# Kernel optimization log

Measured on AMD Instinct MI355X. Metric: run time of the kernel, lower is better.

The kernel has to match this reference:

```python
import jax, jax.numpy as jnp
import numpy as np
import math

B, NOUT, NCLASSES, CENTER, TOPK = 1024, 512, 5994, 3, 5
M, SUB_M, SCALE = 0.2, -0.06, 30.0

COS_M, SIN_M = math.cos(M), math.sin(M)
TH, MM = math.cos(math.pi - M), math.sin(math.pi - M) * M
SUB_COS_M, SUB_SIN_M = math.cos(SUB_M), math.sin(SUB_M)
SUB_TH, SUB_MM = math.cos(math.pi - SUB_M), math.sin(math.pi - SUB_M) * SUB_M


def setup_inputs() -> dict:
    key = jax.random.key(0)
    k1, k2, k3 = jax.random.split(key, 3)
    x = jax.random.normal(k1, (B, NOUT), dtype=jnp.float32)
    # xavier_normal over (center, nClasses, nOut): fan_in=nClasses*nOut, fan_out=center*nOut
    std = math.sqrt(2.0 / (NCLASSES * NOUT + CENTER * NOUT))
    weight = jax.random.normal(k2, (CENTER, NCLASSES, NOUT), dtype=jnp.float32) * std
    label = jax.random.randint(k3, (B,), 0, NCLASSES, dtype=jnp.int64)
    return {"x": x, "weight": weight, "label": label}


def _l2norm(v, axis=-1, eps=1e-12):
    return v / jnp.maximum(jnp.linalg.norm(v, axis=axis, keepdims=True), eps)


def reference(x, weight, label):
    xn = _l2norm(x)                       # [B, j]
    wn = _l2norm(weight)                  # [a, c, j]
    cosine_subcen = jnp.einsum('bj,acj->bac', xn, wn)   # [B, center, C]
    cosine = jnp.max(cosine_subcen, axis=1)             # [B, C]

    sine = jnp.sqrt(jnp.clip(1.0 - cosine * cosine, 0.0, 1.0))
    phi = jnp.where(cosine - TH > 0, cosine * COS_M - sine * SIN_M, cosine - MM)
    sub_phi = jnp.where(cosine - SUB_TH > 0,
                        cosine * SUB_COS_M - sine * SUB_SIN_M,
                        cosine - SUB_MM)

    # topk+1 candidates; drop the label column if present, else drop the last
    _, idx = jax.lax.top_k(cosine, TOPK + 1)            # [B, topk+1]
    is_label = (idx == label[:, None].astype(idx.dtype))
    # stable sort pushes the (unique) label hit to the end, preserving order otherwise
    order = jnp.argsort(is_label.astype(jnp.int32), axis=1, stable=True)
    idx_fixed = jnp.take_along_axis(idx, order[:, :TOPK], axis=1)   # [B, topk]

    rows = jnp.arange(B)[:, None]
    one_hot_sub = jnp.zeros_like(cosine).at[rows, idx_fixed].add(1.0)
    one_hot = jax.nn.one_hot(label, NCLASSES, dtype=cosine.dtype)

    output = (one_hot * phi + one_hot_sub * sub_phi
              + (1.0 - one_hot_sub - one_hot) * cosine) * SCALE

    logp = jax.nn.log_softmax(output, axis=-1)
    loss = -jnp.mean(logp[jnp.arange(B), label])

    pred = jnp.argmax(cosine * SCALE, axis=-1)
    prec1 = jnp.mean((pred == label).astype(jnp.float32)) * 100.0
    return loss, prec1
```

## Files before the change

kernel.cpp:

```cpp
#include <hip/hip_runtime.h>
#include <math.h>

#define NB 1024
#define NC 5994
#define NCP 6016
#define NK 512
#define NA 3
#define NT 48
#define SCALE_F 30.0f
#define NPT 24

#define COS_M_F 0.9800665778412416f
#define SIN_M_F 0.19866933079506122f
#define TH_F (-0.9800665778412416f)
#define MM_F 0.039733866159012244f
#define SUB_COS_M_F 0.9982005399352042f
#define SUB_SIN_M_F (-0.05996400647944459f)
#define SUB_TH_F (-0.9982005399352042f)
#define SUB_MM_F 0.0035978403887666754f

typedef __attribute__((ext_vector_type(8))) short short8;
typedef __attribute__((ext_vector_type(4))) float f32x4;

__device__ __forceinline__ float waveReduceSum(float v) {
#pragma unroll
  for (int off = 32; off > 0; off >>= 1) v += __shfl_down(v, off);
  return v;
}

__device__ __forceinline__ void waveArgMax(float& v, int& i) {
#pragma unroll
  for (int off = 32; off > 0; off >>= 1) {
    float ov = __shfl_down(v, off);
    int oi = __shfl_down(i, off);
    if (ov > v || (ov == v && (unsigned)oi < (unsigned)i)) { v = ov; i = oi; }
  }
}

__device__ __forceinline__ ushort f2bf(float f) {
  unsigned u = __float_as_uint(f);
  u += 0x7FFFu + ((u >> 16) & 1u);
  return (ushort)(u >> 16);
}

__device__ __forceinline__ void load_lds16(const ushort* g, ushort* l) {
  __builtin_amdgcn_global_load_lds(
      (const __attribute__((address_space(1))) unsigned int*)g,
      (__attribute__((address_space(3))) unsigned int*)l, 16, 0, 0);
}

__global__ __launch_bounds__(256) void norm_convert(const float* __restrict__ x,
                                                    const float* __restrict__ w,
                                                    ushort* __restrict__ xb,
                                                    ushort* __restrict__ wb) {
  const int row = blockIdx.x * 4 + (threadIdx.x >> 6);
  const int lane = threadIdx.x & 63;
  const float* src;
  ushort* dst;
  if (row < NB) {
    src = x + (size_t)row * NK;
    dst = xb + (size_t)row * NK;
  } else {
    const int r = row - NB;
    const int a = r / NCP, c = r % NCP;
    dst = wb + (size_t)r * NK;
    if (c >= NC) {
      ushort4 z = {0, 0, 0, 0};
      *(ushort4*)(dst + lane * 4) = z;
      *(ushort4*)(dst + 256 + lane * 4) = z;
      return;
    }
    src = w + ((size_t)a * NC + c) * NK;
  }
  const float4 v0 = *(const float4*)(src + lane * 4);
  const float4 v1 = *(const float4*)(src + 256 + lane * 4);
  float ss = v0.x * v0.x + v0.y * v0.y + v0.z * v0.z + v0.w * v0.w +
             v1.x * v1.x + v1.y * v1.y + v1.z * v1.z + v1.w * v1.w;
  ss = waveReduceSum(ss);
  ss = __shfl(ss, 0);
  const float rn = 1.0f / fmaxf(sqrtf(ss), 1e-12f);
  ushort4 o0 = {f2bf(v0.x * rn), f2bf(v0.y * rn), f2bf(v0.z * rn), f2bf(v0.w * rn)};
  ushort4 o1 = {f2bf(v1.x * rn), f2bf(v1.y * rn), f2bf(v1.z * rn), f2bf(v1.w * rn)};
  *(ushort4*)(dst + lane * 4) = o0;
  *(ushort4*)(dst + 256 + lane * 4) = o1;
}

__global__ __launch_bounds__(256) void cos_gemm_mfma(const ushort* __restrict__ Xb,
                                                     const ushort* __restrict__ Wb,
                                                     float* __restrict__ cosine) {
  __shared__ ushort sA0[128 * 32];
  __shared__ ushort sA1[128 * 32];
  __shared__ ushort sB0[128 * 32];
  __shared__ ushort sB1[128 * 32];
  const int tid = threadIdx.x;
  const int lane = tid & 63;
  const int w = tid >> 6;
  const int wr = w >> 1, wc = w & 1;
  const int b0 = blockIdx.y * 128;
  const int c0 = blockIdx.x * 128;

  const int e0 = w * 2;
  const int srow = e0 * 16 + (lane >> 2);
  const int scol = (lane & 3) * 8;
  const ushort* gA = Xb + (size_t)(b0 + srow) * NK + scol;
  const ushort* gB = Wb + (size_t)(c0 + srow) * NK + scol;
  const int lds0 = e0 * 512;
  const int lds1 = (e0 + 1) * 512;

  const int r = lane & 15;
  const int kg = lane >> 4;
  const int offA = (wr * 64 + r) * 32 + kg * 8;
  const int offB = (wc * 64 + r) * 32 + kg * 8;

  f32x4 best[4][4];
  f32x4 acc[4][4];
#pragma unroll
  for (int i = 0; i < 4; ++i)
#pragma unroll
    for (int j = 0; j < 4; ++j) {
#pragma unroll
      for (int q = 0; q < 4; ++q) best[i][j][q] = -INFINITY;
      acc[i][j] = (f32x4)(0.f);
    }

  load_lds16(gA, (ushort*)sA0 + lds0);
  load_lds16(gA + 16 * NK, (ushort*)sA0 + lds1);
  load_lds16(gB, (ushort*)sB0 + lds0);
  load_lds16(gB + 16 * NK, (ushort*)sB0 + lds1);
  __syncthreads();

#define GEMM_BODY(T, SAr, SBr, SAw, SBw)                                        \
  {                                                                             \
    const int t_ = (T);                                                         \
    if (t_ + 1 < NT) {                                                          \
      const int tn = t_ + 1;                                                    \
      const int k0 = (tn & 15) << 5;                                            \
      const size_t boff = (size_t)(tn >> 4) * NCP * NK;                         \
      load_lds16(gA + k0, (ushort*)SAw + lds0);                                 \
      load_lds16(gA + k0 + 16 * NK, (ushort*)SAw + lds1);                       \
      load_lds16(gB + boff + k0, (ushort*)SBw + lds0);                          \
      load_lds16(gB + boff + k0 + 16 * NK, (ushort*)SBw + lds1);                \
    }                                                                           \
    short8 af[4], bf[4];                                                        \
    _Pragma("unroll") for (int mi = 0; mi < 4; ++mi)                            \
        af[mi] = *(const short8*)&SAr[offA + mi * 512];                         \
    _Pragma("unroll") for (int ni = 0; ni < 4; ++ni)                            \
        bf[ni] = *(const short8*)&SBr[offB + ni * 512];                         \
    _Pragma("unroll") for (int mi = 0; mi < 4; ++mi)                            \
        _Pragma("unroll") for (int ni = 0; ni < 4; ++ni)                        \
            acc[mi][ni] = __builtin_amdgcn_mfma_f32_16x16x32_bf16(              \
                af[mi], bf[ni], acc[mi][ni], 0, 0, 0);                          \
    if ((t_ & 15) == 15) {                                                      \
      _Pragma("unroll") for (int i = 0; i < 4; ++i)                             \
          _Pragma("unroll") for (int j = 0; j < 4; ++j) {                       \
        _Pragma("unroll") for (int q = 0; q < 4; ++q)                           \
            best[i][j][q] = fmaxf(best[i][j][q], acc[i][j][q]);                 \
        acc[i][j] = (f32x4)(0.f);                                               \
      }                                                                         \
    }                                                                           \
    __syncthreads();                                                            \
  }

  for (int t = 0; t < NT; t += 2) {
    GEMM_BODY(t, sA0, sB0, sA1, sB1)
    GEMM_BODY(t + 1, sA1, sB1, sA0, sB0)
  }
#undef GEMM_BODY

  const int q4 = (lane >> 4) * 4;
#pragma unroll
  for (int ni = 0; ni < 4; ++ni) {
    const int col = c0 + wc * 64 + ni * 16 + r;
    if (col < NC) {
#pragma unroll
      for (int mi = 0; mi < 4; ++mi) {
        const int row0 = b0 + wr * 64 + mi * 16 + q4;
#pragma unroll
        for (int q = 0; q < 4; ++q)
          cosine[(size_t)(row0 + q) * NC + col] = best[mi][ni][q];
      }
    }
  }
}

__global__ __launch_bounds__(256) void row_loss(const float* __restrict__ cosine,
                                                const int* __restrict__ label,
                                                float* __restrict__ loss_b,
                                                float* __restrict__ corr_b) {
  __shared__ float swv[4];
  __shared__ int swi[4];
  __shared__ float s_red[4];
  __shared__ float s_maxv;
  __shared__ float s_cosL;
  __shared__ float topv[6];
  __shared__ int topi[6];

  const int b = blockIdx.x, tid = threadIdx.x;
  const int wv = tid >> 6;
  const int lab = label[b];
  const float* row = cosine + (size_t)b * NC;

  float v[NPT];
  float bv = -INFINITY;
  int bi = -1;
#pragma unroll
  for (int j = 0; j < NPT; ++j) {
    const int i = tid + j * 256;
    v[j] = (i < NC) ? row[i] : -INFINITY;
    if (v[j] > bv) { bv = v[j]; bi = i; }
  }
  if (tid == (lab & 255)) s_cosL = v[lab >> 8];
  waveArgMax(bv, bi);
  if ((tid & 63) == 0) { swv[wv] = bv; swi[wv] = bi; }
  __syncthreads();
  if (tid == 0) {
    float mv = swv[0]; int mi = swi[0];
    for (int q = 1; q < 4; ++q)
      if (swv[q] > mv || (swv[q] == mv && (unsigned)swi[q] < (unsigned)mi)) { mv = swv[q]; mi = swi[q]; }
    s_maxv = mv; topv[0] = mv; topi[0] = mi;
  }
  __syncthreads();
  const float maxv = s_maxv;

  float ps = 0.f;
#pragma unroll
  for (int j = 0; j < NPT; ++j) ps += __expf(SCALE_F * (v[j] - maxv));
  ps = waveReduceSum(ps);
  if ((tid & 63) == 0) s_red[wv] = ps;

  unsigned excl = 0;
  {
    const int wi = topi[0];
    if ((wi & 255) == tid) excl |= 1u << (wi >> 8);
  }

  for (int e = 1; e < 6; ++e) {
    float lv = -INFINITY;
    int li = -1;
#pragma unroll
    for (int j = 0; j < NPT; ++j)
      if (!((excl >> j) & 1u) && v[j] > lv) { lv = v[j]; li = tid + j * 256; }
    waveArgMax(lv, li);
    if ((tid & 63) == 0) { swv[wv] = lv; swi[wv] = li; }
    __syncthreads();
    if (tid == 0) {
      float mv = swv[0]; int mi = swi[0];
      for (int q = 1; q < 4; ++q)
        if (swv[q] > mv || (swv[q] == mv && (unsigned)swi[q] < (unsigned)mi)) { mv = swv[q]; mi = swi[q]; }
      topv[e] = mv; topi[e] = mi;
    }
    __syncthreads();
    const int wi = topi[e];
    if ((wi & 255) == tid) excl |= 1u << (wi >> 8);
  }

  if (tid == 0) {
    const float S = s_red[0] + s_red[1] + s_red[2] + s_red[3];
    const float m = SCALE_F * maxv;
    const float cosL = s_cosL;
    const float sineL = sqrtf(fminf(fmaxf(1.f - cosL * cosL, 0.f), 1.f));
    const float phiL = (cosL - TH_F > 0.f) ? (cosL * COS_M_F - sineL * SIN_M_F) : (cosL - MM_F);
    float adj = __expf(SCALE_F * phiL - m) - __expf(SCALE_F * cosL - m);
    int cnt = 0;
    for (int e = 0; e < 6 && cnt < 5; ++e) {
      if (topi[e] == lab) continue;
      const float c = topv[e];
      const float sine = sqrtf(fminf(fmaxf(1.f - c * c, 0.f), 1.f));
      const float sp = (c - SUB_TH_F > 0.f) ? (c * SUB_COS_M_F - sine * SUB_SIN_M_F) : (c - SUB_MM_F);
      adj += __expf(SCALE_F * sp - m) - __expf(SCALE_F * c - m);
      ++cnt;
    }
    const float Sp = S + adj;
    loss_b[b] = (logf(Sp) + m) - SCALE_F * phiL;
    corr_b[b] = (topi[0] == lab) ? 1.f : 0.f;
  }
}

__global__ __launch_bounds__(256) void finalize(const float* __restrict__ loss_b,
                                                const float* __restrict__ corr_b,
                                                float* __restrict__ out) {
  const int tid = threadIdx.x;
  float ls = 0.f, cs = 0.f;
  for (int i = tid; i < NB; i += 256) { ls += loss_b[i]; cs += corr_b[i]; }
  ls = waveReduceSum(ls);
  cs = waveReduceSum(cs);
  __shared__ float sl[4], sc[4];
  if ((tid & 63) == 0) { sl[tid >> 6] = ls; sc[tid >> 6] = cs; }
  __syncthreads();
  if (tid == 0) {
    const float L = sl[0] + sl[1] + sl[2] + sl[3];
    const float Cr = sc[0] + sc[1] + sc[2] + sc[3];
    out[0] = L / (float)NB;
    out[1] = Cr / (float)NB * 100.f;
  }
}

extern "C" void kernel_launch(void* const* d_in, const int* in_sizes, int n_in,
                              void* d_out, int out_size, void* d_ws, size_t ws_size,
                              hipStream_t stream) {
  const float* x = (const float*)d_in[0];
  const float* w = (const float*)d_in[1];
  const int* label = (const int*)d_in[2];
  float* out = (float*)d_out;
  char* ws = (char*)d_ws;

  ushort* xb = (ushort*)ws;
  ushort* wb = (ushort*)(ws + 1048576);
  float* cosine = (float*)(ws + 1048576 + 18481152);
  float* loss_b = (float*)(ws + 1048576 + 18481152 + 24551424);
  float* corr_b = loss_b + NB;

  norm_convert<<<(NB + NA * NCP) / 4, 256, 0, stream>>>(x, w, xb, wb);
  cos_gemm_mfma<<<dim3(NCP / 128, NB / 128), 256, 0, stream>>>(xb, wb, cosine);
  row_loss<<<NB, 256, 0, stream>>>(cosine, label, loss_b, corr_b);
  finalize<<<1, 256, 0, stream>>>(loss_b, corr_b, out);
}
```

Before: 71.90 us.

## Use 512-thread GEMM blocks with swizzled 1D grid and padded classes

The GEMM block grows to 8 waves, each now computing a 32x64 sub-tile instead of 64x64, which halves per-thread accumulators and staging loads. Class padding becomes 6144 so the grid is exactly 48x8 tiles. Blocks are remapped from a 1D grid so that groups of 8 column tiles share row tiles, aimed at better L2 reuse. Loss scratch buffers now reuse the xb workspace region, which is dead by the time row_loss runs. The aim is more latency hiding and fewer registers, at the cost of extra padded rows in normalization and GEMM.

```diff
diff --git a/kernel.cpp b/kernel.cpp
--- a/kernel.cpp
+++ b/kernel.cpp
@@ -3,7 +3,9 @@
 
 #define NB 1024
 #define NC 5994
-#define NCP 6016
+#define NCP 6144
+#define NCX 48
+#define NBY 8
 #define NK 512
 #define NA 3
 #define NT 48
@@ -85,7 +87,7 @@
   *(ushort4*)(dst + 256 + lane * 4) = o1;
 }
 
-__global__ __launch_bounds__(256) void cos_gemm_mfma(const ushort* __restrict__ Xb,
+__global__ __launch_bounds__(512) void cos_gemm_mfma(const ushort* __restrict__ Xb,
                                                      const ushort* __restrict__ Wb,
                                                      float* __restrict__ cosine) {
   __shared__ ushort sA0[128 * 32];
@@ -96,26 +98,30 @@
   const int lane = tid & 63;
   const int w = tid >> 6;
   const int wr = w >> 1, wc = w & 1;
-  const int b0 = blockIdx.y * 128;
-  const int c0 = blockIdx.x * 128;
-
-  const int e0 = w * 2;
-  const int srow = e0 * 16 + (lane >> 2);
+
+  const int id = blockIdx.x;
+  const int resid = id & 7;
+  const int by = (id >> 3) & 7;
+  const int chunk = id >> 6;
+  const int cx = chunk * 8 + resid;
+  const int b0 = by * 128;
+  const int c0 = cx * 128;
+
+  const int srow = w * 16 + (lane >> 2);
   const int scol = (lane & 3) * 8;
   const ushort* gA = Xb + (size_t)(b0 + srow) * NK + scol;
   const ushort* gB = Wb + (size_t)(c0 + srow) * NK + scol;
-  const int lds0 = e0 * 512;
-  const int lds1 = (e0 + 1) * 512;
+  const int ldsw = w * 512;
 
   const int r = lane & 15;
   const int kg = lane >> 4;
-  const int offA = (wr * 64 + r) * 32 + kg * 8;
+  const int offA = (wr * 32 + r) * 32 + kg * 8;
   const int offB = (wc * 64 + r) * 32 + kg * 8;
 
-  f32x4 best[4][4];
-  f32x4 acc[4][4];
-#pragma unroll
-  for (int i = 0; i < 4; ++i)
+  f32x4 best[2][4];
+  f32x4 acc[2][4];
+#pragma unroll
+  for (int i = 0; i < 2; ++i)
 #pragma unroll
     for (int j = 0; j < 4; ++j) {
 #pragma unroll
@@ -123,10 +129,8 @@
       acc[i][j] = (f32x4)(0.f);
     }
 
-  load_lds16(gA, (ushort*)sA0 + lds0);
-  load_lds16(gA + 16 * NK, (ushort*)sA0 + lds1);
-  load_lds16(gB, (ushort*)sB0 + lds0);
-  load_lds16(gB + 16 * NK, (ushort*)sB0 + lds1);
+  load_lds16(gA, (ushort*)sA0 + ldsw);
+  load_lds16(gB, (ushort*)sB0 + ldsw);
   __syncthreads();
 
 #define GEMM_BODY(T, SAr, SBr, SAw, SBw)                                        \
@@ -136,22 +140,20 @@
       const int tn = t_ + 1;                                                    \
       const int k0 = (tn & 15) << 5;                                            \
       const size_t boff = (size_t)(tn >> 4) * NCP * NK;                         \
-      load_lds16(gA + k0, (ushort*)SAw + lds0);                                 \
-      load_lds16(gA + k0 + 16 * NK, (ushort*)SAw + lds1);                       \
-      load_lds16(gB + boff + k0, (ushort*)SBw + lds0);                          \
-      load_lds16(gB + boff + k0 + 16 * NK, (ushort*)SBw + lds1);                \
+      load_lds16(gA + k0, (ushort*)SAw + ldsw);                                 \
+      load_lds16(gB + boff + k0, (ushort*)SBw + ldsw);                          \
     }                                                                           \
-    short8 af[4], bf[4];                                                        \
-    _Pragma("unroll") for (int mi = 0; mi < 4; ++mi)                            \
+    short8 af[2], bf[4];                                                        \
+    _Pragma("unroll") for (int mi = 0; mi < 2; ++mi)                            \
         af[mi] = *(const short8*)&SAr[offA + mi * 512];                         \
     _Pragma("unroll") for (int ni = 0; ni < 4; ++ni)                            \
         bf[ni] = *(const short8*)&SBr[offB + ni * 512];                         \
-    _Pragma("unroll") for (int mi = 0; mi < 4; ++mi)                            \
+    _Pragma("unroll") for (int mi = 0; mi < 2; ++mi)                            \
         _Pragma("unroll") for (int ni = 0; ni < 4; ++ni)                        \
             acc[mi][ni] = __builtin_amdgcn_mfma_f32_16x16x32_bf16(              \
                 af[mi], bf[ni], acc[mi][ni], 0, 0, 0);                          \
     if ((t_ & 15) == 15) {                                                      \
-      _Pragma("unroll") for (int i = 0; i < 4; ++i)                             \
+      _Pragma("unroll") for (int i = 0; i < 2; ++i)                             \
           _Pragma("unroll") for (int j = 0; j < 4; ++j) {                       \
         _Pragma("unroll") for (int q = 0; q < 4; ++q)                           \
             best[i][j][q] = fmaxf(best[i][j][q], acc[i][j][q]);                 \
@@ -173,8 +175,8 @@
     const int col = c0 + wc * 64 + ni * 16 + r;
     if (col < NC) {
 #pragma unroll
-      for (int mi = 0; mi < 4; ++mi) {
-        const int row0 = b0 + wr * 64 + mi * 16 + q4;
+      for (int mi = 0; mi < 2; ++mi) {
+        const int row0 = b0 + wr * 32 + mi * 16 + q4;
 #pragma unroll
         for (int q = 0; q < 4; ++q)
           cosine[(size_t)(row0 + q) * NC + col] = best[mi][ni][q];
@@ -306,12 +308,12 @@
 
   ushort* xb = (ushort*)ws;
   ushort* wb = (ushort*)(ws + 1048576);
-  float* cosine = (float*)(ws + 1048576 + 18481152);
-  float* loss_b = (float*)(ws + 1048576 + 18481152 + 24551424);
-  float* corr_b = loss_b + NB;
+  float* cosine = (float*)(ws + 1048576 + 18874368);
+  float* loss_b = (float*)ws;
+  float* corr_b = (float*)(ws + 4096);
 
   norm_convert<<<(NB + NA * NCP) / 4, 256, 0, stream>>>(x, w, xb, wb);
-  cos_gemm_mfma<<<dim3(NCP / 128, NB / 128), 256, 0, stream>>>(xb, wb, cosine);
+  cos_gemm_mfma<<<NBY * NCX, 512, 0, stream>>>(xb, wb, cosine);
   row_loss<<<NB, 256, 0, stream>>>(cosine, label, loss_b, corr_b);
   finalize<<<1, 256, 0, stream>>>(loss_b, corr_b, out);
 }
```

After: 80.17 us. 11.5% more time.

## Shrink GEMM tile to 64x128 with two waves and swizzle block order

Applied to the files above, without the earlier changes.

The cosine GEMM now uses 64x128 tiles computed by two waves per block instead of 128x128 tiles with four waves. Blocks are launched on a 1D grid with a swizzled mapping that groups eight class tiles per batch-tile sweep, to improve L2 reuse. The class dimension is padded to 6144 so the tiles divide evenly, and the per-row loss buffers are moved into the bf16 x buffer, which is no longer needed by then. The goal is more blocks for better load balance across CUs, at the cost of half the A reuse per block and more redundant W loads.

```diff
diff --git a/kernel.cpp b/kernel.cpp
--- a/kernel.cpp
+++ b/kernel.cpp
@@ -3,7 +3,7 @@
 
 #define NB 1024
 #define NC 5994
-#define NCP 6016
+#define NCP 6144
 #define NK 512
 #define NA 3
 #define NT 48
@@ -85,32 +85,36 @@
   *(ushort4*)(dst + 256 + lane * 4) = o1;
 }
 
-__global__ __launch_bounds__(256) void cos_gemm_mfma(const ushort* __restrict__ Xb,
+__global__ __launch_bounds__(128) void cos_gemm_mfma(const ushort* __restrict__ Xb,
                                                      const ushort* __restrict__ Wb,
                                                      float* __restrict__ cosine) {
-  __shared__ ushort sA0[128 * 32];
-  __shared__ ushort sA1[128 * 32];
+  __shared__ ushort sA0[64 * 32];
+  __shared__ ushort sA1[64 * 32];
   __shared__ ushort sB0[128 * 32];
   __shared__ ushort sB1[128 * 32];
   const int tid = threadIdx.x;
   const int lane = tid & 63;
   const int w = tid >> 6;
-  const int wr = w >> 1, wc = w & 1;
-  const int b0 = blockIdx.y * 128;
-  const int c0 = blockIdx.x * 128;
-
-  const int e0 = w * 2;
-  const int srow = e0 * 16 + (lane >> 2);
-  const int scol = (lane & 3) * 8;
-  const ushort* gA = Xb + (size_t)(b0 + srow) * NK + scol;
-  const ushort* gB = Wb + (size_t)(c0 + srow) * NK + scol;
-  const int lds0 = e0 * 512;
-  const int lds1 = (e0 + 1) * 512;
+
+  const int id = blockIdx.x;
+  const int resid = id & 7;
+  const int by = (id >> 3) & 15;
+  const int chunk = id >> 7;
+  const int cx = chunk * 8 + resid;
+  const int b0 = by * 64;
+  const int c0 = cx * 128;
+
+  const int lrow = lane >> 2;
+  const int lcol8 = (lane & 3) * 8;
+  const ushort* gA = Xb + (size_t)(b0 + 32 * w + lrow) * NK + lcol8;
+  const ushort* gB = Wb + (size_t)(c0 + 64 * w + lrow) * NK + lcol8;
+  const int ldsA = w * 1024;
+  const int ldsB = w * 2048;
 
   const int r = lane & 15;
   const int kg = lane >> 4;
-  const int offA = (wr * 64 + r) * 32 + kg * 8;
-  const int offB = (wc * 64 + r) * 32 + kg * 8;
+  const int offA = r * 32 + kg * 8;
+  const int offB = (w * 64 + r) * 32 + kg * 8;
 
   f32x4 best[4][4];
   f32x4 acc[4][4];
@@ -123,10 +127,11 @@
       acc[i][j] = (f32x4)(0.f);
     }
 
-  load_lds16(gA, (ushort*)sA0 + lds0);
-  load_lds16(gA + 16 * NK, (ushort*)sA0 + lds1);
-  load_lds16(gB, (ushort*)sB0 + lds0);
-  load_lds16(gB + 16 * NK, (ushort*)sB0 + lds1);
+  load_lds16(gA, (ushort*)sA0 + ldsA);
+  load_lds16(gA + 16 * NK, (ushort*)sA0 + ldsA + 512);
+#pragma unroll
+  for (int j = 0; j < 4; ++j)
+    load_lds16(gB + j * 16 * NK, (ushort*)sB0 + ldsB + j * 512);
   __syncthreads();
 
 #define GEMM_BODY(T, SAr, SBr, SAw, SBw)                                        \
@@ -136,10 +141,11 @@
       const int tn = t_ + 1;                                                    \
       const int k0 = (tn & 15) << 5;                                            \
       const size_t boff = (size_t)(tn >> 4) * NCP * NK;                         \
-      load_lds16(gA + k0, (ushort*)SAw + lds0);                                 \
-      load_lds16(gA + k0 + 16 * NK, (ushort*)SAw + lds1);                       \
-      load_lds16(gB + boff + k0, (ushort*)SBw + lds0);                          \
-      load_lds16(gB + boff + k0 + 16 * NK, (ushort*)SBw + lds1);                \
+      load_lds16(gA + k0, (ushort*)SAw + ldsA);                                 \
+      load_lds16(gA + k0 + 16 * NK, (ushort*)SAw + ldsA + 512);                 \
+      _Pragma("unroll") for (int j = 0; j < 4; ++j)                             \
+          load_lds16(gB + boff + k0 + j * 16 * NK,                              \
+                     (ushort*)SBw + ldsB + j * 512);                            \
     }                                                                           \
     short8 af[4], bf[4];                                                        \
     _Pragma("unroll") for (int mi = 0; mi < 4; ++mi)                            \
@@ -170,11 +176,11 @@
   const int q4 = (lane >> 4) * 4;
 #pragma unroll
   for (int ni = 0; ni < 4; ++ni) {
-    const int col = c0 + wc * 64 + ni * 16 + r;
+    const int col = c0 + w * 64 + ni * 16 + r;
     if (col < NC) {
 #pragma unroll
       for (int mi = 0; mi < 4; ++mi) {
-        const int row0 = b0 + wr * 64 + mi * 16 + q4;
+        const int row0 = b0 + mi * 16 + q4;
 #pragma unroll
         for (int q = 0; q < 4; ++q)
           cosine[(size_t)(row0 + q) * NC + col] = best[mi][ni][q];
@@ -306,12 +312,12 @@
 
   ushort* xb = (ushort*)ws;
   ushort* wb = (ushort*)(ws + 1048576);
-  float* cosine = (float*)(ws + 1048576 + 18481152);
-  float* loss_b = (float*)(ws + 1048576 + 18481152 + 24551424);
-  float* corr_b = loss_b + NB;
+  float* cosine = (float*)(ws + 1048576 + 18874368);
+  float* loss_b = (float*)ws;
+  float* corr_b = (float*)(ws + 4096);
 
   norm_convert<<<(NB + NA * NCP) / 4, 256, 0, stream>>>(x, w, xb, wb);
-  cos_gemm_mfma<<<dim3(NCP / 128, NB / 128), 256, 0, stream>>>(xb, wb, cosine);
+  cos_gemm_mfma<<<16 * 48, 128, 0, stream>>>(xb, wb, cosine);
   row_loss<<<NB, 256, 0, stream>>>(cosine, label, loss_b, corr_b);
   finalize<<<1, 256, 0, stream>>>(loss_b, corr_b, out);
 }
```

After: 68.10 us. -5.3%, faster.
